# Performance work log

Hardware: AMD Instinct MI355X
Metric: run time of the kernel (lower is better)

## Reference

```python
import jax, jax.numpy as jnp
import numpy as np

N_WAY = 5
NKPTS = 17
EMBED = 512
N_SUPPORT = 25  # 5-way 5-shot
N_QUERY = 65536


def setup_inputs() -> dict:
    key = jax.random.key(0)
    ks = jax.random.split(key, 12)
    def lin(k, fan_in, fan_out):
        return jax.random.normal(k, (fan_in, fan_out), jnp.float32) / np.float32(np.sqrt(fan_in))
    return {
        'support_features': jax.random.normal(ks[0], (1, N_SUPPORT, EMBED), jnp.float32),
        'support_keypoints': jax.random.uniform(ks[1], (N_SUPPORT, NKPTS, 2), jnp.float32),
        'query_features': jax.random.normal(ks[2], (N_QUERY, EMBED), jnp.float32),
        'image_coords': jax.random.uniform(ks[3], (N_QUERY, 2), jnp.float32) * 512.0,
        'W1': lin(ks[4], EMBED, EMBED), 'b1': jnp.zeros((EMBED,), jnp.float32),
        'W2': lin(ks[5], EMBED, EMBED), 'b2': jnp.zeros((EMBED,), jnp.float32),
        'Wo1': lin(ks[6], EMBED, EMBED // 2), 'bo1': jnp.zeros((EMBED // 2,), jnp.float32),
        'Wo2': lin(ks[7], EMBED // 2, 2), 'bo2': jnp.zeros((2,), jnp.float32),
        'Wc1': lin(ks[8], EMBED, EMBED // 2), 'bc1': jnp.zeros((EMBED // 2,), jnp.float32),
        'Wc2': lin(ks[9], EMBED // 2, 1), 'bc2': jnp.zeros((1,), jnp.float32),
        'temperature': jnp.float32(1.0),
    }


def reference(support_features, support_keypoints, query_features, image_coords,
              W1, b1, W2, b2, Wo1, bo1, Wo2, bo2, Wc1, bc1, Wc2, bc2, temperature):
    eps = 1e-8
    nkpts = support_keypoints.shape[1]
    n_query = query_features.shape[0]
    D = query_features.shape[-1]

    # --- compute_prototypes (batch_size == 1; per-kpt prototype identical by construction) ---
    sf = support_features.reshape(-1, D)                      # [Ns, D]
    h = jnp.maximum(sf @ W1 + b1, 0.0) @ W2 + b2              # prototype_net MLP
    n_per = h.shape[0] // N_WAY
    proto_way = h.reshape(N_WAY, n_per, D).mean(axis=1)       # [n_way, D]
    prototypes = jnp.broadcast_to(proto_way[:, None, :], (N_WAY, nkpts, D))

    # --- compute_distances: 1 - cosine_sim, scaled by temperature ---
    qn = jnp.linalg.norm(query_features, axis=-1)             # [Nq]
    pn = jnp.linalg.norm(proto_way, axis=-1)                  # [n_way]
    sim = (query_features @ proto_way.T) / jnp.maximum(qn[:, None] * pn[None, :], eps)
    dist_way = (1.0 - sim) / temperature                      # [Nq, n_way]
    distances = jnp.broadcast_to(dist_way[:, :, None], (n_query, N_WAY, nkpts))

    # --- predict_keypoints ---
    # avg over kpts is a no-op (identical per kpt); argmin over ways
    class_predictions = jnp.argmin(dist_way, axis=1)          # [Nq] int
    # softmax over a single scalar == 1.0, so keypoints == offset broadcast over kpts
    offset = jnp.maximum(query_features @ Wo1 + bo1, 0.0) @ Wo2 + bo2   # [Nq, 2]
    conf = jax.nn.sigmoid(jnp.maximum(query_features @ Wc1 + bc1, 0.0) @ Wc2 + bc2)  # [Nq, 1]
    keypoints = jnp.broadcast_to(offset[:, None, :], (n_query, nkpts, 2))
    keypoints = jax.nn.sigmoid(keypoints) * image_coords[:, None, :]    # image_coords provided
    confidence = jnp.broadcast_to(conf, (n_query, nkpts))

    return keypoints, confidence, distances, class_predictions, prototypes
```

## Files before the change

### kernel.cpp

```cpp
#include <hip/hip_runtime.h>
#include <hip/hip_bf16.h>

#define NQ 65536
#define DIM 512
#define HID 256
#define NWAY 5
#define NKPTS 17

typedef short bf16x8 __attribute__((ext_vector_type(8)));
typedef float f32x4 __attribute__((ext_vector_type(4)));
typedef _Float16 half8 __attribute__((ext_vector_type(8)));

static __device__ __forceinline__ unsigned short f2bf(float f) {
    unsigned int x = __float_as_uint(f);
    unsigned int r = (x + 0x7fffu + ((x >> 16) & 1u)) >> 16;
    return (unsigned short)r;
}

static __device__ __forceinline__ void async16(void* l, const void* g) {
    __builtin_amdgcn_global_load_lds(
        (const __attribute__((address_space(1))) unsigned int*)g,
        (__attribute__((address_space(3))) unsigned int*)l, 16, 0, 0);
}

__global__ __launch_bounds__(256) void k_sup(const float* __restrict__ sf,
                                             const float* __restrict__ W1, const float* __restrict__ b1,
                                             float* __restrict__ ws_h1) {
    __shared__ float sfl[512];
    __shared__ float red[4][64];
    int bx = blockIdx.x;
    int s = bx >> 3, cb = bx & 7;
    int t = threadIdx.x;
    if (t < 128) ((float4*)sfl)[t] = ((const float4*)(sf + s * DIM))[t];
    __syncthreads();
    int c = cb * 64 + (t & 63);
    int qd = t >> 6;
    const float* Wp = W1 + (size_t)qd * 128 * DIM + c;
    float acc = 0.0f;
    #pragma unroll 4
    for (int kk = 0; kk < 128; kk++)
        acc += sfl[qd * 128 + kk] * Wp[(size_t)kk * DIM];
    red[qd][t & 63] = acc;
    __syncthreads();
    if (t < 64) {
        float h = red[0][t] + red[1][t] + red[2][t] + red[3][t] + b1[cb * 64 + t];
        ws_h1[s * DIM + cb * 64 + t] = fmaxf(h, 0.0f);
    }
}

__global__ __launch_bounds__(256) void k_mid2(const float* __restrict__ ws_h1,
                                              const float* __restrict__ W2, const float* __restrict__ b2,
                                              const float* __restrict__ Wo1, const float* __restrict__ Wc1,
                                              float* __restrict__ ws_proto, unsigned short* __restrict__ wb) {
    int bx = blockIdx.x;
    int t = threadIdx.x;
    if (bx < 40) {
        __shared__ float ml[512];
        __shared__ float red[4][64];
        int w = bx >> 3, cb = bx & 7;
        for (int i = t; i < 512; i += 256) {
            float sum = 0.0f;
            #pragma unroll
            for (int s5 = 0; s5 < 5; s5++) sum += ws_h1[(w * 5 + s5) * DIM + i];
            ml[i] = sum * 0.2f;
        }
        __syncthreads();
        int c = cb * 64 + (t & 63);
        int qd = t >> 6;
        const float* Wp = W2 + (size_t)qd * 128 * DIM + c;
        float acc = 0.0f;
        #pragma unroll 4
        for (int kk = 0; kk < 128; kk++)
            acc += ml[qd * 128 + kk] * Wp[(size_t)kk * DIM];
        red[qd][t & 63] = acc;
        __syncthreads();
        if (t < 64)
            ws_proto[w * DIM + cb * 64 + t] =
                red[0][t] + red[1][t] + red[2][t] + red[3][t] + b2[cb * 64 + t];
    } else {
        __shared__ unsigned short T[64][72];
        int tb = bx - 40;
        const float* src = (tb < 32) ? Wo1 : Wc1;
        int cofs = (tb < 32) ? 0 : 256;
        int tt = tb & 31;
        int kt = tt >> 2;
        int ct = tt & 3;
        int i = t >> 2;
        int qd = t & 3;
        const float* rp = src + (size_t)(kt * 64 + i) * HID + ct * 64 + qd * 16;
        #pragma unroll
        for (int v = 0; v < 4; v++) {
            float4 x = *(const float4*)(rp + v * 4);
            T[qd * 16 + v * 4 + 0][i] = f2bf(x.x);
            T[qd * 16 + v * 4 + 1][i] = f2bf(x.y);
            T[qd * 16 + v * 4 + 2][i] = f2bf(x.z);
            T[qd * 16 + v * 4 + 3][i] = f2bf(x.w);
        }
        __syncthreads();
        int j = t >> 2;
        int part = t & 3;
        uint4 o0 = *(const uint4*)&T[j][part * 16];
        uint4 o1 = *(const uint4*)&T[j][part * 16 + 8];
        unsigned short* dst = wb + (size_t)(cofs + ct * 64 + j) * DIM + kt * 64 + part * 16;
        *(uint4*)dst = o0;
        *(uint4*)(dst + 8) = o1;
    }
}

__global__ __launch_bounds__(256) void k_prep(const float* __restrict__ qf,
                                              const float* __restrict__ ws_proto,
                                              const float* __restrict__ temp_p,
                                              unsigned short* __restrict__ qbf,
                                              float* __restrict__ out_dist, float* __restrict__ out_class,
                                              float* __restrict__ out_proto) {
    __shared__ float dlds[32 * NWAY];
    int bx = blockIdx.x, t = threadIdx.x;
    int wv = t >> 6, lane = t & 63;

    if (bx < NWAY * NKPTS && t < 128) {
        f32x4 v = *(const f32x4*)(ws_proto + (bx / NKPTS) * DIM + t * 4);
        *(f32x4*)(out_proto + (size_t)bx * DIM + t * 4) = v;
    }

    float p[NWAY][8];
    float pn[NWAY];
    {
        float pp[NWAY];
        #pragma unroll
        for (int w = 0; w < NWAY; w++) {
            f32x4 a = *(const f32x4*)(ws_proto + w * DIM + lane * 8);
            f32x4 b = *(const f32x4*)(ws_proto + w * DIM + lane * 8 + 4);
            p[w][0] = a[0]; p[w][1] = a[1]; p[w][2] = a[2]; p[w][3] = a[3];
            p[w][4] = b[0]; p[w][5] = b[1]; p[w][6] = b[2]; p[w][7] = b[3];
            float s = 0.0f;
            #pragma unroll
            for (int j = 0; j < 8; j++) s += p[w][j] * p[w][j];
            pp[w] = s;
        }
        #pragma unroll
        for (int off = 32; off > 0; off >>= 1) {
            #pragma unroll
            for (int w = 0; w < NWAY; w++) pp[w] += __shfl_xor(pp[w], off, 64);
        }
        #pragma unroll
        for (int w = 0; w < NWAY; w++) pn[w] = sqrtf(pp[w]);
    }
    float invt = 1.0f / temp_p[0];

    int qbase = bx * 32 + wv * 8;
    for (int qi = 0; qi < 8; qi++) {
        int Q = qbase + qi;
        const float* vp = qf + (size_t)Q * DIM + lane * 8;
        float4 v0 = *(const float4*)vp;
        float4 v1 = *(const float4*)(vp + 4);
        unsigned int r0 = f2bf(v0.x) | ((unsigned int)f2bf(v0.y) << 16);
        unsigned int r1 = f2bf(v0.z) | ((unsigned int)f2bf(v0.w) << 16);
        unsigned int r2 = f2bf(v1.x) | ((unsigned int)f2bf(v1.y) << 16);
        unsigned int r3 = f2bf(v1.z) | ((unsigned int)f2bf(v1.w) << 16);
        *(uint4*)(qbf + (size_t)Q * DIM + lane * 8) = make_uint4(r0, r1, r2, r3);

        float av[8] = {v0.x, v0.y, v0.z, v0.w, v1.x, v1.y, v1.z, v1.w};
        float d[NWAY + 1];
        #pragma unroll
        for (int w = 0; w < NWAY; w++) {
            float s = 0.0f;
            #pragma unroll
            for (int j = 0; j < 8; j++) s += av[j] * p[w][j];
            d[w] = s;
        }
        {
            float s = 0.0f;
            #pragma unroll
            for (int j = 0; j < 8; j++) s += av[j] * av[j];
            d[NWAY] = s;
        }
        #pragma unroll
        for (int off = 32; off > 0; off >>= 1) {
            #pragma unroll
            for (int k2 = 0; k2 < NWAY + 1; k2++) d[k2] += __shfl_xor(d[k2], off, 64);
        }
        float qn = sqrtf(d[NWAY]);
        float mv = 1e30f; int ami = 0;
        float d0, d1c, d2c, d3c, d4c;
        {
            float dist[NWAY];
            #pragma unroll
            for (int w = 0; w < NWAY; w++) {
                float den = fmaxf(qn * pn[w], 1e-8f);
                float dd = (1.0f - d[w] / den) * invt;
                dist[w] = dd;
                if (dd < mv) { mv = dd; ami = w; }
            }
            d0 = dist[0]; d1c = dist[1]; d2c = dist[2]; d3c = dist[3]; d4c = dist[4];
        }
        if (lane == 0) {
            out_class[Q] = (float)ami;
            int b0 = (wv * 8 + qi) * NWAY;
            dlds[b0 + 0] = d0; dlds[b0 + 1] = d1c; dlds[b0 + 2] = d2c;
            dlds[b0 + 3] = d3c; dlds[b0 + 4] = d4c;
        }
    }
    __syncthreads();
    int Q0 = bx * 32;
    for (int i = t; i < 32 * NWAY * NKPTS; i += 256) {
        int q2 = i / (NWAY * NKPTS);
        int rem = i - q2 * (NWAY * NKPTS);
        out_dist[(size_t)(Q0 + q2) * (NWAY * NKPTS) + rem] = dlds[q2 * NWAY + rem / NKPTS];
    }
}

__global__ __launch_bounds__(512) void k_gemm(const unsigned short* __restrict__ qbf,
                                              const unsigned short* __restrict__ wb,
                                              const float* __restrict__ bo1, const float* __restrict__ Wo2,
                                              const float* __restrict__ bo2,
                                              const float* __restrict__ bc1, const float* __restrict__ Wc2,
                                              const float* __restrict__ bc2,
                                              const float* __restrict__ ic,
                                              float* __restrict__ out_kp, float* __restrict__ out_conf) {
    __shared__ __align__(16) char smem[98304];
    unsigned short* Ab = (unsigned short*)smem;
    unsigned short* Bb = (unsigned short*)(smem + 32768);

    int bx = blockIdx.x;
    int mb = bx >> 1, nb = bx & 1;
    int t = threadIdx.x;
    int wv = t >> 6, lane = t & 63;
    int wr = wv >> 2, wc = wv & 3;
    int r = lane & 15, hq = lane >> 4;

    int lrow = lane >> 3;
    int lslot = (lane & 7) ^ lrow;
    const unsigned short* Ag = qbf + (size_t)mb * (128 * DIM) + (size_t)lrow * DIM + lslot * 8;
    const unsigned short* Bg = wb + (size_t)nb * (HID * DIM) + (size_t)lrow * DIM + lslot * 8;

    f32x4 acc[4][4];
    #pragma unroll
    for (int i2 = 0; i2 < 4; i2++)
        #pragma unroll
        for (int j2 = 0; j2 < 4; j2++) { f32x4 z = {0.0f, 0.0f, 0.0f, 0.0f}; acc[i2][j2] = z; }

    #pragma unroll
    for (int i = 0; i < 2; i++) {
        int ci = wv * 2 + i;
        async16(smem + ci * 1024, Ag + (size_t)ci * 8 * DIM);
    }
    #pragma unroll
    for (int i = 0; i < 4; i++) {
        int ci = wv * 4 + i;
        async16(smem + 32768 + ci * 1024, Bg + (size_t)ci * 8 * DIM);
    }
    __syncthreads();

    for (int it = 0; it < 8; it++) {
        int par = it & 1;
        if (it < 7) {
            int ko = (it + 1) * 64;
            int pn2 = par ^ 1;
            #pragma unroll
            for (int i = 0; i < 2; i++) {
                int ci = wv * 2 + i;
                async16(smem + pn2 * 16384 + ci * 1024, Ag + (size_t)ci * 8 * DIM + ko);
            }
            #pragma unroll
            for (int i = 0; i < 4; i++) {
                int ci = wv * 4 + i;
                async16(smem + 32768 + pn2 * 32768 + ci * 1024, Bg + (size_t)ci * 8 * DIM + ko);
            }
        }
        const unsigned short* Ap = Ab + par * 8192;
        const unsigned short* Bp = Bb + par * 16384;
        #pragma unroll
        for (int ks = 0; ks < 2; ks++) {
            int slot = ks * 4 + hq;
            bf16x8 af[4], bfr[4];
            #pragma unroll
            for (int mt = 0; mt < 4; mt++) {
                int m = wr * 64 + mt * 16 + r;
                af[mt] = *(const bf16x8*)(Ap + m * 64 + ((slot ^ (m & 7)) * 8));
            }
            #pragma unroll
            for (int nt = 0; nt < 4; nt++) {
                int c = wc * 64 + nt * 16 + r;
                bfr[nt] = *(const bf16x8*)(Bp + c * 64 + ((slot ^ (c & 7)) * 8));
            }
            #pragma unroll
            for (int mt = 0; mt < 4; mt++)
                #pragma unroll
                for (int nt = 0; nt < 4; nt++)
                    acc[mt][nt] = __builtin_amdgcn_mfma_f32_16x16x32_bf16(af[mt], bfr[nt], acc[mt][nt], 0, 0, 0);
        }
        __syncthreads();
    }

    const float* bias = nb ? bc1 : bo1;
    _Float16* hl = (_Float16*)smem;
    #pragma unroll
    for (int nt = 0; nt < 4; nt++) {
        int cl = wc * 64 + nt * 16 + r;
        float bv = bias[cl];
        #pragma unroll
        for (int mt = 0; mt < 4; mt++)
            #pragma unroll
            for (int rg = 0; rg < 4; rg++) {
                int ml = wr * 64 + mt * 16 + hq * 4 + rg;
                hl[ml * 264 + cl] = (_Float16)fmaxf(acc[mt][nt][rg] + bv, 0.0f);
            }
    }
    __syncthreads();

    float* redf = (float*)(smem + 128 * 264 * 2);
    int q = t & 127, qt = t >> 7;
    if (nb == 0) {
        float ox = 0.0f, oy = 0.0f;
        #pragma unroll 2
        for (int j0 = 0; j0 < 64; j0 += 8) {
            half8 hv = *(const half8*)(hl + q * 264 + qt * 64 + j0);
            #pragma unroll
            for (int j = 0; j < 8; j++) {
                float2 w2 = *(const float2*)(Wo2 + (qt * 64 + j0 + j) * 2);
                float hf = (float)hv[j];
                ox += hf * w2.x;
                oy += hf * w2.y;
            }
        }
        redf[(qt * 128 + q) * 2] = ox;
        redf[(qt * 128 + q) * 2 + 1] = oy;
        __syncthreads();
        if (t < 128) {
            float sx = bo2[0], sy = bo2[1];
            #pragma unroll
            for (int k2 = 0; k2 < 4; k2++) {
                sx += redf[(k2 * 128 + t) * 2];
                sy += redf[(k2 * 128 + t) * 2 + 1];
            }
            size_t Q = (size_t)mb * 128 + t;
            float2 icv = *(const float2*)(ic + Q * 2);
            float gx = icv.x / (1.0f + __expf(-sx));
            float gy = icv.y / (1.0f + __expf(-sy));
            float2 g2 = make_float2(gx, gy);
            float2* dst = (float2*)(out_kp + Q * 34);
            #pragma unroll
            for (int k2 = 0; k2 < 17; k2++) dst[k2] = g2;
        }
    } else {
        float cs = 0.0f;
        #pragma unroll 2
        for (int j0 = 0; j0 < 64; j0 += 8) {
            half8 hv = *(const half8*)(hl + q * 264 + qt * 64 + j0);
            #pragma unroll
            for (int j = 0; j < 8; j++)
                cs += (float)hv[j] * Wc2[qt * 64 + j0 + j];
        }
        redf[qt * 128 + q] = cs;
        __syncthreads();
        if (t < 128) {
            float s = bc2[0] + redf[t] + redf[128 + t] + redf[256 + t] + redf[384 + t];
            float sg = 1.0f / (1.0f + __expf(-s));
            size_t Q = (size_t)mb * 128 + t;
            float* dst = out_conf + Q * 17;
            #pragma unroll
            for (int k2 = 0; k2 < 17; k2++) dst[k2] = sg;
        }
    }
}

extern "C" void kernel_launch(void* const* d_in, const int* in_sizes, int n_in,
                              void* d_out, int out_size, void* d_ws, size_t ws_size,
                              hipStream_t stream) {
    const float* sf = (const float*)d_in[0];
    const float* qf = (const float*)d_in[2];
    const float* ic = (const float*)d_in[3];
    const float* W1 = (const float*)d_in[4];
    const float* b1 = (const float*)d_in[5];
    const float* W2 = (const float*)d_in[6];
    const float* b2 = (const float*)d_in[7];
    const float* Wo1 = (const float*)d_in[8];
    const float* bo1 = (const float*)d_in[9];
    const float* Wo2 = (const float*)d_in[10];
    const float* bo2 = (const float*)d_in[11];
    const float* Wc1 = (const float*)d_in[12];
    const float* bc1 = (const float*)d_in[13];
    const float* Wc2 = (const float*)d_in[14];
    const float* bc2 = (const float*)d_in[15];
    const float* temp = (const float*)d_in[16];

    float* out = (float*)d_out;
    float* out_kp = out;
    float* out_conf = out + 2228224;
    float* out_dist = out + 3342336;
    float* out_class = out + 8912896;
    float* out_proto = out + 8978432;

    char* ws = (char*)d_ws;
    float* ws_h1 = (float*)ws;
    float* ws_proto = (float*)(ws + 51200);
    unsigned short* ws_wb = (unsigned short*)(ws + 65536);
    unsigned short* ws_qbf = (unsigned short*)(ws + 1048576);

    hipLaunchKernelGGL(k_sup, dim3(200), dim3(256), 0, stream, sf, W1, b1, ws_h1);
    hipLaunchKernelGGL(k_mid2, dim3(104), dim3(256), 0, stream, ws_h1, W2, b2, Wo1, Wc1, ws_proto, ws_wb);
    hipLaunchKernelGGL(k_prep, dim3(2048), dim3(256), 0, stream, qf, ws_proto, temp,
                       ws_qbf, out_dist, out_class, out_proto);
    hipLaunchKernelGGL(k_gemm, dim3(1024), dim3(512), 0, stream, ws_qbf, ws_wb,
                       bo1, Wo2, bo2, bc1, Wc2, bc2, ic, out_kp, out_conf);
}
```

Measured before the change: 335.8 us.

## Compute both heads per block with 128x512 tile and batch prep reductions

The GEMM kernel now has each block compute all 512 output columns (offset and confidence heads together) for 128 queries. It uses a K-step of 32 and 8 N-tiles per wave, so the A tile is loaded once instead of twice and half as many blocks launch. The epilogue runs the two heads one after the other, reusing the same LDS region. Separately, the prep kernel batches the shuffle reductions for its 8 queries and spreads the finalisation across 8 lanes, which should expose more ILP. The cost is more accumulator registers (128 floats per thread), which may reduce occupancy, and more K iterations with a barrier in each.

```diff
diff --git a/kernel.cpp b/kernel.cpp
--- a/kernel.cpp
+++ b/kernel.cpp
@@ -148,56 +148,56 @@
     float invt = 1.0f / temp_p[0];
 
     int qbase = bx * 32 + wv * 8;
+    const float* qp = qf + (size_t)qbase * DIM + lane * 8;
+    unsigned short* qb = qbf + (size_t)qbase * DIM + lane * 8;
+
+    float dq[8][NWAY + 1];
+    #pragma unroll
     for (int qi = 0; qi < 8; qi++) {
-        int Q = qbase + qi;
-        const float* vp = qf + (size_t)Q * DIM + lane * 8;
-        float4 v0 = *(const float4*)vp;
-        float4 v1 = *(const float4*)(vp + 4);
+        float4 v0 = *(const float4*)(qp + qi * DIM);
+        float4 v1 = *(const float4*)(qp + qi * DIM + 4);
         unsigned int r0 = f2bf(v0.x) | ((unsigned int)f2bf(v0.y) << 16);
         unsigned int r1 = f2bf(v0.z) | ((unsigned int)f2bf(v0.w) << 16);
         unsigned int r2 = f2bf(v1.x) | ((unsigned int)f2bf(v1.y) << 16);
         unsigned int r3 = f2bf(v1.z) | ((unsigned int)f2bf(v1.w) << 16);
-        *(uint4*)(qbf + (size_t)Q * DIM + lane * 8) = make_uint4(r0, r1, r2, r3);
-
+        *(uint4*)(qb + qi * DIM) = make_uint4(r0, r1, r2, r3);
         float av[8] = {v0.x, v0.y, v0.z, v0.w, v1.x, v1.y, v1.z, v1.w};
-        float d[NWAY + 1];
         #pragma unroll
         for (int w = 0; w < NWAY; w++) {
             float s = 0.0f;
             #pragma unroll
             for (int j = 0; j < 8; j++) s += av[j] * p[w][j];
-            d[w] = s;
-        }
-        {
-            float s = 0.0f;
-            #pragma unroll
-            for (int j = 0; j < 8; j++) s += av[j] * av[j];
-            d[NWAY] = s;
-        }
-        #pragma unroll
-        for (int off = 32; off > 0; off >>= 1) {
-            #pragma unroll
-            for (int k2 = 0; k2 < NWAY + 1; k2++) d[k2] += __shfl_xor(d[k2], off, 64);
-        }
-        float qn = sqrtf(d[NWAY]);
-        float mv = 1e30f; int ami = 0;
-        float d0, d1c, d2c, d3c, d4c;
-        {
-            float dist[NWAY];
-            #pragma unroll
-            for (int w = 0; w < NWAY; w++) {
-                float den = fmaxf(qn * pn[w], 1e-8f);
-                float dd = (1.0f - d[w] / den) * invt;
-                dist[w] = dd;
-                if (dd < mv) { mv = dd; ami = w; }
+            dq[qi][w] = s;
+        }
+        float s = 0.0f;
+        #pragma unroll
+        for (int j = 0; j < 8; j++) s += av[j] * av[j];
+        dq[qi][NWAY] = s;
+    }
+    #pragma unroll
+    for (int off = 32; off > 0; off >>= 1) {
+        #pragma unroll
+        for (int qi = 0; qi < 8; qi++) {
+            #pragma unroll
+            for (int j = 0; j < NWAY + 1; j++)
+                dq[qi][j] += __shfl_xor(dq[qi][j], off, 64);
+        }
+    }
+    if (lane < 8) {
+        #pragma unroll
+        for (int qi = 0; qi < 8; qi++) {
+            if (lane == qi) {
+                float qn = sqrtf(dq[qi][NWAY]);
+                float mv = 1e30f; int ami = 0;
+                #pragma unroll
+                for (int w = 0; w < NWAY; w++) {
+                    float den = fmaxf(qn * pn[w], 1e-8f);
+                    float dd = (1.0f - dq[qi][w] / den) * invt;
+                    dlds[(wv * 8 + qi) * NWAY + w] = dd;
+                    if (dd < mv) { mv = dd; ami = w; }
+                }
+                out_class[qbase + qi] = (float)ami;
             }
-            d0 = dist[0]; d1c = dist[1]; d2c = dist[2]; d3c = dist[3]; d4c = dist[4];
-        }
-        if (lane == 0) {
-            out_class[Q] = (float)ami;
-            int b0 = (wv * 8 + qi) * NWAY;
-            dlds[b0 + 0] = d0; dlds[b0 + 1] = d1c; dlds[b0 + 2] = d2c;
-            dlds[b0 + 3] = d3c; dlds[b0 + 4] = d4c;
         }
     }
     __syncthreads();
@@ -217,100 +217,85 @@
                                               const float* __restrict__ bc2,
                                               const float* __restrict__ ic,
                                               float* __restrict__ out_kp, float* __restrict__ out_conf) {
-    __shared__ __align__(16) char smem[98304];
-    unsigned short* Ab = (unsigned short*)smem;
-    unsigned short* Bb = (unsigned short*)(smem + 32768);
-
-    int bx = blockIdx.x;
-    int mb = bx >> 1, nb = bx & 1;
+    __shared__ __align__(16) char smem[81920];
+    char* Abase = smem;
+    char* Bbase = smem + 16384;
+
+    int mb = blockIdx.x;
     int t = threadIdx.x;
     int wv = t >> 6, lane = t & 63;
     int wr = wv >> 2, wc = wv & 3;
     int r = lane & 15, hq = lane >> 4;
 
-    int lrow = lane >> 3;
-    int lslot = (lane & 7) ^ lrow;
-    const unsigned short* Ag = qbf + (size_t)mb * (128 * DIM) + (size_t)lrow * DIM + lslot * 8;
-    const unsigned short* Bg = wb + (size_t)nb * (HID * DIM) + (size_t)lrow * DIM + lslot * 8;
-
-    f32x4 acc[4][4];
+    int srow = lane >> 2;
+    int sg = (lane & 3) ^ (srow & 3);
+    const unsigned short* Ag = qbf + ((size_t)mb * 128 + wv * 16 + srow) * DIM + sg * 8;
+    const unsigned short* Bg = wb + ((size_t)wv * 64 + srow) * DIM + sg * 8;
+
+    f32x4 acc[4][8];
     #pragma unroll
     for (int i2 = 0; i2 < 4; i2++)
         #pragma unroll
-        for (int j2 = 0; j2 < 4; j2++) { f32x4 z = {0.0f, 0.0f, 0.0f, 0.0f}; acc[i2][j2] = z; }
-
+        for (int j2 = 0; j2 < 8; j2++) { f32x4 z = {0.0f, 0.0f, 0.0f, 0.0f}; acc[i2][j2] = z; }
+
+    async16(Abase + wv * 1024, Ag);
     #pragma unroll
-    for (int i = 0; i < 2; i++) {
-        int ci = wv * 2 + i;
-        async16(smem + ci * 1024, Ag + (size_t)ci * 8 * DIM);
-    }
-    #pragma unroll
-    for (int i = 0; i < 4; i++) {
-        int ci = wv * 4 + i;
-        async16(smem + 32768 + ci * 1024, Bg + (size_t)ci * 8 * DIM);
-    }
-    __syncthreads();
-
-    for (int it = 0; it < 8; it++) {
+    for (int i = 0; i < 4; i++)
+        async16(Bbase + wv * 4096 + i * 1024, Bg + (size_t)i * 16 * DIM);
+    __syncthreads();
+
+    for (int it = 0; it < 16; it++) {
         int par = it & 1;
-        if (it < 7) {
-            int ko = (it + 1) * 64;
-            int pn2 = par ^ 1;
-            #pragma unroll
-            for (int i = 0; i < 2; i++) {
-                int ci = wv * 2 + i;
-                async16(smem + pn2 * 16384 + ci * 1024, Ag + (size_t)ci * 8 * DIM + ko);
-            }
-            #pragma unroll
-            for (int i = 0; i < 4; i++) {
-                int ci = wv * 4 + i;
-                async16(smem + 32768 + pn2 * 32768 + ci * 1024, Bg + (size_t)ci * 8 * DIM + ko);
-            }
-        }
-        const unsigned short* Ap = Ab + par * 8192;
-        const unsigned short* Bp = Bb + par * 16384;
-        #pragma unroll
-        for (int ks = 0; ks < 2; ks++) {
-            int slot = ks * 4 + hq;
-            bf16x8 af[4], bfr[4];
-            #pragma unroll
-            for (int mt = 0; mt < 4; mt++) {
-                int m = wr * 64 + mt * 16 + r;
-                af[mt] = *(const bf16x8*)(Ap + m * 64 + ((slot ^ (m & 7)) * 8));
-            }
-            #pragma unroll
-            for (int nt = 0; nt < 4; nt++) {
-                int c = wc * 64 + nt * 16 + r;
-                bfr[nt] = *(const bf16x8*)(Bp + c * 64 + ((slot ^ (c & 7)) * 8));
-            }
+        if (it < 15) {
+            int ko = (it + 1) * 32;
+            int np = par ^ 1;
+            async16(Abase + np * 8192 + wv * 1024, Ag + ko);
+            #pragma unroll
+            for (int i = 0; i < 4; i++)
+                async16(Bbase + np * 32768 + wv * 4096 + i * 1024, Bg + (size_t)i * 16 * DIM + ko);
+        }
+        const unsigned short* Ap = (const unsigned short*)(Abase + par * 8192);
+        const unsigned short* Bp = (const unsigned short*)(Bbase + par * 32768);
+        int sl = (hq ^ (r & 3)) * 8;
+        bf16x8 af[4], bfr[8];
+        #pragma unroll
+        for (int mt = 0; mt < 4; mt++) {
+            int m = wr * 64 + mt * 16 + r;
+            af[mt] = *(const bf16x8*)(Ap + m * 32 + sl);
+        }
+        #pragma unroll
+        for (int nt = 0; nt < 8; nt++) {
+            int c = wc * 128 + nt * 16 + r;
+            bfr[nt] = *(const bf16x8*)(Bp + c * 32 + sl);
+        }
+        #pragma unroll
+        for (int mt = 0; mt < 4; mt++)
+            #pragma unroll
+            for (int nt = 0; nt < 8; nt++)
+                acc[mt][nt] = __builtin_amdgcn_mfma_f32_16x16x32_bf16(af[mt], bfr[nt], acc[mt][nt], 0, 0, 0);
+        __syncthreads();
+    }
+
+    _Float16* hl = (_Float16*)smem;
+    float* redf = (float*)(smem + 67584);
+
+    if (wc < 2) {
+        #pragma unroll
+        for (int nt = 0; nt < 8; nt++) {
+            int cl = wc * 128 + nt * 16 + r;
+            float bv = bo1[cl];
             #pragma unroll
             for (int mt = 0; mt < 4; mt++)
                 #pragma unroll
-                for (int nt = 0; nt < 4; nt++)
-                    acc[mt][nt] = __builtin_amdgcn_mfma_f32_16x16x32_bf16(af[mt], bfr[nt], acc[mt][nt], 0, 0, 0);
-        }
-        __syncthreads();
-    }
-
-    const float* bias = nb ? bc1 : bo1;
-    _Float16* hl = (_Float16*)smem;
-    #pragma unroll
-    for (int nt = 0; nt < 4; nt++) {
-        int cl = wc * 64 + nt * 16 + r;
-        float bv = bias[cl];
-        #pragma unroll
-        for (int mt = 0; mt < 4; mt++)
-            #pragma unroll
-            for (int rg = 0; rg < 4; rg++) {
-                int ml = wr * 64 + mt * 16 + hq * 4 + rg;
-                hl[ml * 264 + cl] = (_Float16)fmaxf(acc[mt][nt][rg] + bv, 0.0f);
-            }
-    }
-    __syncthreads();
-
-    float* redf = (float*)(smem + 128 * 264 * 2);
-    int q = t & 127, qt = t >> 7;
-    if (nb == 0) {
+                for (int rg = 0; rg < 4; rg++) {
+                    int ml = wr * 64 + mt * 16 + hq * 4 + rg;
+                    hl[ml * 264 + cl] = (_Float16)fmaxf(acc[mt][nt][rg] + bv, 0.0f);
+                }
+        }
+    }
+    __syncthreads();
+    {
+        int q = t & 127, qt = t >> 7;
         float ox = 0.0f, oy = 0.0f;
         #pragma unroll 2
         for (int j0 = 0; j0 < 64; j0 += 8) {
@@ -325,24 +310,41 @@
         }
         redf[(qt * 128 + q) * 2] = ox;
         redf[(qt * 128 + q) * 2 + 1] = oy;
-        __syncthreads();
-        if (t < 128) {
-            float sx = bo2[0], sy = bo2[1];
-            #pragma unroll
-            for (int k2 = 0; k2 < 4; k2++) {
-                sx += redf[(k2 * 128 + t) * 2];
-                sy += redf[(k2 * 128 + t) * 2 + 1];
-            }
-            size_t Q = (size_t)mb * 128 + t;
-            float2 icv = *(const float2*)(ic + Q * 2);
-            float gx = icv.x / (1.0f + __expf(-sx));
-            float gy = icv.y / (1.0f + __expf(-sy));
-            float2 g2 = make_float2(gx, gy);
-            float2* dst = (float2*)(out_kp + Q * 34);
-            #pragma unroll
-            for (int k2 = 0; k2 < 17; k2++) dst[k2] = g2;
-        }
-    } else {
+    }
+    __syncthreads();
+    if (t < 128) {
+        float sx = bo2[0], sy = bo2[1];
+        #pragma unroll
+        for (int k2 = 0; k2 < 4; k2++) {
+            sx += redf[(k2 * 128 + t) * 2];
+            sy += redf[(k2 * 128 + t) * 2 + 1];
+        }
+        size_t Q = (size_t)mb * 128 + t;
+        float2 icv = *(const float2*)(ic + Q * 2);
+        float gx = icv.x / (1.0f + __expf(-sx));
+        float gy = icv.y / (1.0f + __expf(-sy));
+        float2 g2 = make_float2(gx, gy);
+        float2* dst = (float2*)(out_kp + Q * 34);
+        #pragma unroll
+        for (int k2 = 0; k2 < 17; k2++) dst[k2] = g2;
+    }
+    if (wc >= 2) {
+        #pragma unroll
+        for (int nt = 0; nt < 8; nt++) {
+            int cl = (wc - 2) * 128 + nt * 16 + r;
+            float bv = bc1[cl];
+            #pragma unroll
+            for (int mt = 0; mt < 4; mt++)
+                #pragma unroll
+                for (int rg = 0; rg < 4; rg++) {
+                    int ml = wr * 64 + mt * 16 + hq * 4 + rg;
+                    hl[ml * 264 + cl] = (_Float16)fmaxf(acc[mt][nt][rg] + bv, 0.0f);
+                }
+        }
+    }
+    __syncthreads();
+    {
+        int q = t & 127, qt = t >> 7;
         float cs = 0.0f;
         #pragma unroll 2
         for (int j0 = 0; j0 < 64; j0 += 8) {
@@ -352,15 +354,15 @@
                 cs += (float)hv[j] * Wc2[qt * 64 + j0 + j];
         }
         redf[qt * 128 + q] = cs;
-        __syncthreads();
-        if (t < 128) {
-            float s = bc2[0] + redf[t] + redf[128 + t] + redf[256 + t] + redf[384 + t];
-            float sg = 1.0f / (1.0f + __expf(-s));
-            size_t Q = (size_t)mb * 128 + t;
-            float* dst = out_conf + Q * 17;
-            #pragma unroll
-            for (int k2 = 0; k2 < 17; k2++) dst[k2] = sg;
-        }
+    }
+    __syncthreads();
+    if (t < 128) {
+        float s = bc2[0] + redf[t] + redf[128 + t] + redf[256 + t] + redf[384 + t];
+        float sg2 = 1.0f / (1.0f + __expf(-s));
+        size_t Q = (size_t)mb * 128 + t;
+        float* dst = out_conf + Q * 17;
+        #pragma unroll
+        for (int k2 = 0; k2 < 17; k2++) dst[k2] = sg2;
     }
 }
 
@@ -401,6 +403,6 @@
     hipLaunchKernelGGL(k_mid2, dim3(104), dim3(256), 0, stream, ws_h1, W2, b2, Wo1, Wc1, ws_proto, ws_wb);
     hipLaunchKernelGGL(k_prep, dim3(2048), dim3(256), 0, stream, qf, ws_proto, temp,
                        ws_qbf, out_dist, out_class, out_proto);
-    hipLaunchKernelGGL(k_gemm, dim3(1024), dim3(512), 0, stream, ws_qbf, ws_wb,
+    hipLaunchKernelGGL(k_gemm, dim3(512), dim3(512), 0, stream, ws_qbf, ws_wb,
                        bo1, Wo2, bo2, bc1, Wc2, bc2, ic, out_kp, out_conf);
 }
```

Measured after the change: 341.0 us. About the same (+1.5%).
